# Optimization experiments

Hardware: AMD Instinct MI355X
Metric: run time of the kernel (lower is better)

## Reference

```python
import jax, jax.numpy as jnp
import numpy as np

GAMMA = 0.9  # decay (init kwarg)


def setup_inputs() -> dict:
    key = jax.random.key(0)
    k0, k1, k2, k3 = jax.random.split(key, 4)
    B, T, D = 16, 2048, 256
    x = jax.random.normal(k0, (B, T, D), jnp.float32)
    scale = 1.0 / np.sqrt(D)
    Wq = jax.random.normal(k1, (D, D), jnp.float32) * scale
    Wk = jax.random.normal(k2, (D, D), jnp.float32) * scale
    Wv = jax.random.normal(k3, (D, D), jnp.float32) * scale
    return {"x": x, "Wq": Wq, "Wk": Wk, "Wv": Wv}


def reference(x, Wq, Wk, Wv):
    # x: [B, T, D]
    B, T, D = x.shape
    Q = x @ Wq  # [B, T, D]
    K = x @ Wk
    V = x @ Wv

    # Sequential retention recurrence over the [D, D] state:
    #   s[t] = gamma * s[t-1] + K[:, t, :]^T @ V[:, t, :]   (sums over batch, as in source)
    Kt = jnp.swapaxes(K, 0, 1)  # [T, B, D]
    Vt = jnp.swapaxes(V, 0, 1)  # [T, B, D]

    def step(s, kv):
        k_t, v_t = kv  # each [B, D]
        s = GAMMA * s + k_t.T @ v_t  # [D, D]
        return s, s.sum(-1)  # emit row-sum [D]

    # Loop runs t = 1 .. T-1 in the source (s starts at 0); s[0] := s[1].
    init = jnp.zeros((D, D), x.dtype)
    _, rows = jax.lax.scan(step, init, (Kt[1:], Vt[1:]))  # rows: [T-1, D]
    S = jnp.concatenate([rows[:1], rows], axis=0)  # [T, D]

    # Faithful to tf.reshape(S, [-1, seq_len]) then tf.transpose: a reshape-scramble,
    # NOT a plain transpose of S.
    S2 = S.reshape(D, T).T  # [T, D]
    return S2[None, :, :] * Q  # broadcast over batch -> [B, T, D]
```

## Files before the change

### kernel.cpp

```cpp
#include <hip/hip_runtime.h>
#include <hip/hip_bf16.h>
#include <math.h>


#define GAMMA_F 0.9f
#define T_LEN 2048
#define D_DIM 256
#define B_DIM 16

typedef __attribute__((ext_vector_type(8))) short bf16x8;
typedef __attribute__((ext_vector_type(16))) float f32x16;

__device__ inline ushort f2bf(float f) {
    union { float f; unsigned u; } v; v.f = f;
    unsigned r = (v.u + 0x7FFFu + ((v.u >> 16) & 1u)) >> 16;
    return (ushort)r;
}

__global__ __launch_bounds__(256) void k_prep(const float* __restrict__ Wq,
                                              const float* __restrict__ Wk,
                                              const float* __restrict__ Wv,
                                              ushort* __restrict__ WqT,
                                              ushort* __restrict__ WkT,
                                              float* __restrict__ wv_sum) {
    int bid = blockIdx.x;
    int tid = threadIdx.x;
    if (bid < 32) {
        __shared__ float tile[64][68];
        const float* W = (bid < 16) ? Wq : Wk;
        ushort* WT = (bid < 16) ? WqT : WkT;
        int b = bid & 15;
        int k0 = (b & 3) * 64;
        int n0 = (b >> 2) * 64;
        int r = tid >> 4;
        int c4 = (tid & 15) * 4;
#pragma unroll
        for (int i = 0; i < 4; ++i) {
            float4 v = *(const float4*)(W + (size_t)(k0 + r + 16 * i) * D_DIM + n0 + c4);
            *(float4*)&tile[r + 16 * i][c4] = v;
        }
        __syncthreads();
        int n = tid >> 2;
        int j0 = (tid & 3) * 16;
        ushort tmp[16];
#pragma unroll
        for (int i = 0; i < 16; ++i) tmp[i] = f2bf(tile[j0 + i][n]);
        ushort* dst = WT + (size_t)(n0 + n) * D_DIM + k0 + j0;
#pragma unroll
        for (int i = 0; i < 16; ++i) dst[i] = tmp[i];
    } else {
        int j = (bid - 32) * 64 + (tid >> 2);
        int q = tid & 3;
        const float4* row4 = (const float4*)(Wv + (size_t)j * D_DIM + q * 64);
        float s = 0.f;
#pragma unroll
        for (int i = 0; i < 16; ++i) {
            float4 v = row4[i];
            s += v.x + v.y + v.z + v.w;
        }
        s += __shfl_xor(s, 1, 64);
        s += __shfl_xor(s, 2, 64);
        if (q == 0) wv_sum[j] = s;
    }
}

__global__ __launch_bounds__(256) void k_y(const float* __restrict__ x,
                                           const float* __restrict__ wv_sum,
                                           ushort* __restrict__ ybf) {
    int t = blockIdx.x;
    int d = threadIdx.x;
    float wvd = wv_sum[d];
    float xr[B_DIM];
#pragma unroll
    for (int b = 0; b < B_DIM; ++b)
        xr[b] = x[((size_t)b * T_LEN + t) * D_DIM + d];

    __shared__ float red[B_DIM][4];
    int wave = d >> 6, lane = d & 63;
#pragma unroll
    for (int b = 0; b < B_DIM; ++b) {
        float p = xr[b] * wvd;
        for (int o = 32; o > 0; o >>= 1) p += __shfl_down(p, o, 64);
        if (lane == 0) red[b][wave] = p;
    }
    __syncthreads();
    float yv = 0.f;
#pragma unroll
    for (int b = 0; b < B_DIM; ++b) {
        float wb = red[b][0] + red[b][1] + red[b][2] + red[b][3];
        yv += wb * xr[b];
    }
    ybf[(size_t)t * D_DIM + d] = f2bf(yv);
}

__global__ __launch_bounds__(256) void k_gs(const ushort* __restrict__ ybf,
                                            const ushort* __restrict__ WkT,
                                            float* __restrict__ loc,
                                            float* __restrict__ carry) {
    __shared__ ushort As[32 * 64 * 8];
    __shared__ ushort Bs[32 * 64 * 8];
    float* Cs = (float*)As;
    int mt = blockIdx.x >> 2;
    int nt = blockIdx.x & 3;
    int tid = threadIdx.x, lane = tid & 63, w = tid >> 6;
    int wr = w >> 1, wc = w & 1, l31 = lane & 31, lh = lane >> 5;

#pragma unroll
    for (int i = 0; i < 8; ++i) {
        int slot = tid + 256 * i;
        int r = slot >> 5;
        int s2h = slot & 31;
        int rs = r ^ (s2h & 7);
        *(bf16x8*)&As[(s2h * 64 + rs) * 8] =
            *(const bf16x8*)&ybf[(size_t)(mt * 64 + r) * D_DIM + s2h * 8];
        *(bf16x8*)&Bs[(s2h * 64 + rs) * 8] =
            *(const bf16x8*)&WkT[(size_t)(nt * 64 + r) * D_DIM + s2h * 8];
    }
    __syncthreads();

    f32x16 acc;
#pragma unroll
    for (int e = 0; e < 16; ++e) acc[e] = 0.f;
#pragma unroll
    for (int s = 0; s < 16; ++s) {
        int s2h = s * 2 + lh;
        int ra = (wr * 32 + l31) ^ (s2h & 7);
        int rb = (wc * 32 + l31) ^ (s2h & 7);
        bf16x8 a = *(bf16x8*)&As[(s2h * 64 + ra) * 8];
        bf16x8 b = *(bf16x8*)&Bs[(s2h * 64 + rb) * 8];
        acc = __builtin_amdgcn_mfma_f32_32x32x16_bf16(a, b, acc, 0, 0, 0);
    }
    __syncthreads();

#pragma unroll
    for (int reg = 0; reg < 16; ++reg) {
        int rr = (reg & 3) + 8 * (reg >> 2) + 4 * lh;
        Cs[(wr * 32 + rr) * 64 + wc * 32 + l31] = acc[reg];
    }
    __syncthreads();

#pragma unroll
    for (int half = 0; half < 2; ++half) {
        int task = half * 256 + tid;
        int dl = task & 63;
        int cl = task >> 6;
        float a = 0.f;
#pragma unroll
        for (int j = 0; j < 8; ++j) {
            int tl = cl * 8 + j;
            int gt = mt * 64 + tl;
            float v = (gt == 0) ? 0.f : Cs[tl * 64 + dl];
            a = GAMMA_F * a + v;
            loc[(size_t)gt * D_DIM + nt * 64 + dl] = a;
        }
        carry[(size_t)(mt * 8 + cl) * D_DIM + nt * 64 + dl] = a;
    }
}

__global__ __launch_bounds__(256) void k_S2P(const float* __restrict__ loc,
                                             const float* __restrict__ carry,
                                             float* __restrict__ S2) {
    int tp = blockIdx.x;
    int r = threadIdx.x;
    int src = (tp == 0) ? 1 : tp;
    int c = src >> 3, o = src & 7;
    const float g8 = 0.43046721f;
    int j0 = c - 32; if (j0 < 0) j0 = 0;
    float p = 0.f;
    for (int j = j0; j < c; ++j)
        p = p * g8 + carry[(size_t)j * D_DIM + r];
    const float log2g = -0.15200309344504995f;
    float gp = exp2f((float)(o + 1) * log2g);
    float Aval = loc[(size_t)src * D_DIM + r] + gp * p;
    int trow = ((tp & 7) << 8) + r;
    int dcol = tp >> 3;
    S2[(size_t)trow * D_DIM + dcol] = Aval;
}

__global__ __launch_bounds__(256) void k_qgemm(const float* __restrict__ x,
                                               const ushort* __restrict__ WqT,
                                               const float* __restrict__ S2,
                                               float* __restrict__ out) {
    __shared__ ushort As[8 * 128 * 8];
    __shared__ ushort Bs[8 * 128 * 8];
    int bid = blockIdx.x;
    int mb = bid >> 1;
    int nb = bid & 1;
    int tid = threadIdx.x;
    int lane = tid & 63, w = tid >> 6;
    int wr = w >> 1, wc = w & 1;
    int l31 = lane & 31, lh = lane >> 5;

    f32x16 acc[2][2];
#pragma unroll
    for (int i = 0; i < 2; ++i)
#pragma unroll
        for (int j = 0; j < 2; ++j)
#pragma unroll
            for (int e = 0; e < 16; ++e) acc[i][j][e] = 0.f;

    int r = tid >> 1;
    int h0 = tid & 1;
    const float* ag = x + (size_t)(mb * 128 + r) * D_DIM + h0 * 32;
    const ushort* bg = WqT + (size_t)(nb * 128 + r) * D_DIM + h0 * 32;

    for (int kb = 0; kb < 4; ++kb) {
#pragma unroll
        for (int j = 0; j < 4; ++j) {
            float4 v0 = *(const float4*)(ag + kb * 64 + j * 8);
            float4 v1 = *(const float4*)(ag + kb * 64 + j * 8 + 4);
            ushort4 p0, p1;
            p0.x = f2bf(v0.x); p0.y = f2bf(v0.y); p0.z = f2bf(v0.z); p0.w = f2bf(v0.w);
            p1.x = f2bf(v1.x); p1.y = f2bf(v1.y); p1.z = f2bf(v1.z); p1.w = f2bf(v1.w);
            *(ushort4*)&As[((h0 * 4 + j) * 128 + r) * 8] = p0;
            *(ushort4*)&As[((h0 * 4 + j) * 128 + r) * 8 + 4] = p1;
            bf16x8 bv = *(const bf16x8*)(bg + kb * 64 + j * 8);
            *(bf16x8*)&Bs[((h0 * 4 + j) * 128 + r) * 8] = bv;
        }
        __syncthreads();
#pragma unroll
        for (int s = 0; s < 4; ++s) {
            int c0 = (s * 2 + lh) * 128;
            bf16x8 a0 = *(bf16x8*)&As[(c0 + wr * 64 + l31) * 8];
            bf16x8 a1 = *(bf16x8*)&As[(c0 + wr * 64 + 32 + l31) * 8];
            bf16x8 b0 = *(bf16x8*)&Bs[(c0 + wc * 64 + l31) * 8];
            bf16x8 b1 = *(bf16x8*)&Bs[(c0 + wc * 64 + 32 + l31) * 8];
            acc[0][0] = __builtin_amdgcn_mfma_f32_32x32x16_bf16(a0, b0, acc[0][0], 0, 0, 0);
            acc[0][1] = __builtin_amdgcn_mfma_f32_32x32x16_bf16(a0, b1, acc[0][1], 0, 0, 0);
            acc[1][0] = __builtin_amdgcn_mfma_f32_32x32x16_bf16(a1, b0, acc[1][0], 0, 0, 0);
            acc[1][1] = __builtin_amdgcn_mfma_f32_32x32x16_bf16(a1, b1, acc[1][1], 0, 0, 0);
        }
        __syncthreads();
    }

    int t_base = (mb & 15) * 128;
    size_t row_base = (size_t)mb * 128;
#pragma unroll
    for (int mi = 0; mi < 2; ++mi) {
#pragma unroll
        for (int ni = 0; ni < 2; ++ni) {
            int gn = nb * 128 + wc * 64 + ni * 32 + l31;
#pragma unroll
            for (int reg = 0; reg < 16; ++reg) {
                int rr = (reg & 3) + 8 * (reg >> 2) + 4 * lh;
                int m = wr * 64 + mi * 32 + rr;
                float s2v = S2[(size_t)(t_base + m) * D_DIM + gn];
                out[(row_base + m) * D_DIM + gn] = acc[mi][ni][reg] * s2v;
            }
        }
    }
}

extern "C" void kernel_launch(void* const* d_in, const int* in_sizes, int n_in,
                              void* d_out, int out_size, void* d_ws, size_t ws_size,
                              hipStream_t stream) {
    const float* x  = (const float*)d_in[0];
    const float* Wq = (const float*)d_in[1];
    const float* Wk = (const float*)d_in[2];
    const float* Wv = (const float*)d_in[3];
    float* out = (float*)d_out;

    float* ws = (float*)d_ws;
    float* loc    = ws;
    float* S2     = loc + 524288;
    float* wv_sum = S2 + 524288;
    float* carry  = wv_sum + 256;
    ushort* WqT   = (ushort*)(carry + 65536);
    ushort* WkT   = WqT + 65536;
    ushort* ybf   = WkT + 65536;

    k_prep<<<36, 256, 0, stream>>>(Wq, Wk, Wv, WqT, WkT, wv_sum);
    k_y<<<T_LEN, 256, 0, stream>>>(x, wv_sum, ybf);
    k_gs<<<128, 256, 0, stream>>>(ybf, WkT, loc, carry);
    k_S2P<<<T_LEN, 256, 0, stream>>>(loc, carry, S2);
    k_qgemm<<<(B_DIM * T_LEN / 128) * 2, 256, 0, stream>>>(x, WqT, S2, out);
}
```

Baseline: 128.6 us.

## Precast x to bf16 in k_y, use direct-to-LDS loads in qgemm, coalesce S2 writes

k_y now also writes a bf16 copy of x, since it already reads every element. k_qgemm then loads bf16 A and B tiles straight into LDS with global_load_lds, instead of converting fp32 x in registers and storing to LDS. k_S2P is restructured into 64 blocks that each compute a 32-column strip and stage it through shared memory, so S2 gets coalesced float4 writes in place of strided scalar writes. This adds a 16 MB bf16 write of x and its re-read, but halves the bytes the GEMM reads from x and removes the scattered S2 stores.

```diff
diff --git a/kernel.cpp b/kernel.cpp
--- a/kernel.cpp
+++ b/kernel.cpp
@@ -1,5 +1,4 @@
 #include <hip/hip_runtime.h>
-#include <hip/hip_bf16.h>
 #include <math.h>
 
 
@@ -15,6 +14,12 @@
     union { float f; unsigned u; } v; v.f = f;
     unsigned r = (v.u + 0x7FFFu + ((v.u >> 16) & 1u)) >> 16;
     return (ushort)r;
+}
+
+__device__ __forceinline__ void gload_lds16(const void* g, void* l) {
+    __builtin_amdgcn_global_load_lds(
+        (const __attribute__((address_space(1))) unsigned int*)g,
+        (__attribute__((address_space(3))) unsigned int*)l, 16, 0, 0);
 }
 
 __global__ __launch_bounds__(256) void k_prep(const float* __restrict__ Wq,
@@ -66,7 +71,8 @@
 
 __global__ __launch_bounds__(256) void k_y(const float* __restrict__ x,
                                            const float* __restrict__ wv_sum,
-                                           ushort* __restrict__ ybf) {
+                                           ushort* __restrict__ ybf,
+                                           ushort* __restrict__ xbf) {
     int t = blockIdx.x;
     int d = threadIdx.x;
     float wvd = wv_sum[d];
@@ -74,6 +80,10 @@
 #pragma unroll
     for (int b = 0; b < B_DIM; ++b)
         xr[b] = x[((size_t)b * T_LEN + t) * D_DIM + d];
+
+#pragma unroll
+    for (int b = 0; b < B_DIM; ++b)
+        xbf[((size_t)b * T_LEN + t) * D_DIM + d] = f2bf(xr[b]);
 
     __shared__ float red[B_DIM][4];
     int wave = d >> 6, lane = d & 63;
@@ -160,24 +170,45 @@
 __global__ __launch_bounds__(256) void k_S2P(const float* __restrict__ loc,
                                              const float* __restrict__ carry,
                                              float* __restrict__ S2) {
-    int tp = blockIdx.x;
+    __shared__ float Ls[256][33];
+    int o = blockIdx.x >> 3;
+    int dseg = blockIdx.x & 7;
     int r = threadIdx.x;
-    int src = (tp == 0) ? 1 : tp;
-    int c = src >> 3, o = src & 7;
+    int dstart = dseg * 32;
     const float g8 = 0.43046721f;
-    int j0 = c - 32; if (j0 < 0) j0 = 0;
-    float p = 0.f;
-    for (int j = j0; j < c; ++j)
-        p = p * g8 + carry[(size_t)j * D_DIM + r];
     const float log2g = -0.15200309344504995f;
     float gp = exp2f((float)(o + 1) * log2g);
-    float Aval = loc[(size_t)src * D_DIM + r] + gp * p;
-    int trow = ((tp & 7) << 8) + r;
-    int dcol = tp >> 3;
-    S2[(size_t)trow * D_DIM + dcol] = Aval;
-}
-
-__global__ __launch_bounds__(256) void k_qgemm(const float* __restrict__ x,
+
+    float p = 0.f;
+    int j0 = dstart - 32; if (j0 < 0) j0 = 0;
+    for (int j = j0; j < dstart; ++j)
+        p = p * g8 + carry[(size_t)j * D_DIM + r];
+
+#pragma unroll
+    for (int dd = 0; dd < 32; ++dd) {
+        int d_ = dstart + dd;
+        float Aval = loc[(size_t)(8 * d_ + o) * D_DIM + r] + gp * p;
+        if (o == 0 && d_ == 0) Aval = loc[D_DIM + r];
+        Ls[r][dd] = Aval;
+        p = p * g8 + carry[(size_t)d_ * D_DIM + r];
+    }
+    __syncthreads();
+
+    int rr = threadIdx.x >> 3;
+    int cq = threadIdx.x & 7;
+#pragma unroll
+    for (int it = 0; it < 8; ++it) {
+        int row = it * 32 + rr;
+        float4 v;
+        v.x = Ls[row][cq * 4 + 0];
+        v.y = Ls[row][cq * 4 + 1];
+        v.z = Ls[row][cq * 4 + 2];
+        v.w = Ls[row][cq * 4 + 3];
+        *(float4*)&S2[(size_t)((o << 8) + row) * D_DIM + dstart + cq * 4] = v;
+    }
+}
+
+__global__ __launch_bounds__(256) void k_qgemm(const ushort* __restrict__ xbf,
                                                const ushort* __restrict__ WqT,
                                                const float* __restrict__ S2,
                                                float* __restrict__ out) {
@@ -199,23 +230,18 @@
 #pragma unroll
             for (int e = 0; e < 16; ++e) acc[i][j][e] = 0.f;
 
-    int r = tid >> 1;
-    int h0 = tid & 1;
-    const float* ag = x + (size_t)(mb * 128 + r) * D_DIM + h0 * 32;
-    const ushort* bg = WqT + (size_t)(nb * 128 + r) * D_DIM + h0 * 32;
+    const ushort* ab = xbf + (size_t)mb * 128 * D_DIM;
+    const ushort* bb = WqT + (size_t)nb * 128 * D_DIM;
 
     for (int kb = 0; kb < 4; ++kb) {
 #pragma unroll
-        for (int j = 0; j < 4; ++j) {
-            float4 v0 = *(const float4*)(ag + kb * 64 + j * 8);
-            float4 v1 = *(const float4*)(ag + kb * 64 + j * 8 + 4);
-            ushort4 p0, p1;
-            p0.x = f2bf(v0.x); p0.y = f2bf(v0.y); p0.z = f2bf(v0.z); p0.w = f2bf(v0.w);
-            p1.x = f2bf(v1.x); p1.y = f2bf(v1.y); p1.z = f2bf(v1.z); p1.w = f2bf(v1.w);
-            *(ushort4*)&As[((h0 * 4 + j) * 128 + r) * 8] = p0;
-            *(ushort4*)&As[((h0 * 4 + j) * 128 + r) * 8 + 4] = p1;
-            bf16x8 bv = *(const bf16x8*)(bg + kb * 64 + j * 8);
-            *(bf16x8*)&Bs[((h0 * 4 + j) * 128 + r) * 8] = bv;
+        for (int i = 0; i < 4; ++i) {
+            int slot = i * 256 + tid;
+            int kk = slot >> 7;
+            int row = slot & 127;
+            int ldsbase = (i * 256 + w * 64) * 8;
+            gload_lds16(ab + (size_t)row * D_DIM + kb * 64 + kk * 8, &As[ldsbase]);
+            gload_lds16(bb + (size_t)row * D_DIM + kb * 64 + kk * 8, &Bs[ldsbase]);
         }
         __syncthreads();
 #pragma unroll
@@ -268,10 +294,11 @@
     ushort* WqT   = (ushort*)(carry + 65536);
     ushort* WkT   = WqT + 65536;
     ushort* ybf   = WkT + 65536;
+    ushort* xbf   = ybf + 524288;
 
     k_prep<<<36, 256, 0, stream>>>(Wq, Wk, Wv, WqT, WkT, wv_sum);
-    k_y<<<T_LEN, 256, 0, stream>>>(x, wv_sum, ybf);
+    k_y<<<T_LEN, 256, 0, stream>>>(x, wv_sum, ybf, xbf);
     k_gs<<<128, 256, 0, stream>>>(ybf, WkT, loc, carry);
-    k_S2P<<<T_LEN, 256, 0, stream>>>(loc, carry, S2);
-    k_qgemm<<<(B_DIM * T_LEN / 128) * 2, 256, 0, stream>>>(x, WqT, S2, out);
-}
+    k_S2P<<<64, 256, 0, stream>>>(loc, carry, S2);
+    k_qgemm<<<(B_DIM * T_LEN / 128) * 2, 256, 0, stream>>>(xbf, WqT, S2, out);
+}
```

Measured after the change: 130.8 us. About the same (+1.7%).
